# Kernel optimization log

Measured on AMD Instinct MI355X. Metric: run time of the kernel, lower is better.

Reference implementation:

```python
import jax, jax.numpy as jnp
import numpy as np

N, M, Q, H, T = 4096, 64, 64, 64, 4  # atoms, neighbors/atom, dim_q, num_neurons, num_types
BOX_L = 10.0


def setup_inputs() -> dict:
    key = jax.random.key(0)
    ks = jax.random.split(key, 7)
    return {
        "descriptors": jax.random.normal(ks[0], (N, Q), jnp.float32),
        "gradients": jax.random.normal(ks[1], (N, M, 3, Q), jnp.float32) * 0.1,
        "positions": jax.random.uniform(ks[2], (N, 3), jnp.float32) * BOX_L,
        "box": jnp.eye(3, dtype=jnp.float32) * BOX_L,
        "W0": jax.random.normal(ks[3], (T, Q, H), jnp.float32) * (1.0 / np.sqrt(Q)),
        "b0": jnp.zeros((T, H), jnp.float32),
        "W1": jax.random.normal(ks[4], (T, H), jnp.float32) * (1.0 / np.sqrt(H)),
        "Z": jax.random.randint(ks[5], (N,), 0, T, dtype=jnp.int32),
        "grad_index": jax.random.randint(ks[6], (N, M), 0, N, dtype=jnp.int32),
    }


def _pairwise_rij2(positions, box):
    """Minimum-image squared pairwise distances [N, N] (diagonal masked later)."""
    inv_box = jnp.linalg.inv(box)
    d = positions[None, :, :] - positions[:, None, :]   # [N, N, 3]
    s = d @ inv_box
    s = s - jnp.round(s)
    d = s @ box
    return jnp.sum(d * d, axis=-1)                      # [N, N] = rij^2


def reference(descriptors, gradients, positions, box, W0, b0, W1, Z, grad_index):
    n = descriptors.shape[0]
    # per-type weight gather
    W0_t = W0[Z]            # [N, Q, H]
    b0_t = b0[Z]            # [N, H]
    W1_t = W1[Z]            # [N, H]
    # hidden activations
    h = jnp.tanh(jnp.einsum('nq,nqh->nh', descriptors, W0_t) + b0_t)  # [N, H]
    # chain rule: dU_i/dq = ((1 - h^2) * W1_t) @ W0_t^T
    de_dq = jnp.einsum('nh,nqh->nq', (1.0 - h * h) * W1_t, W0_t)      # [N, Q]
    # forces: dU_i/dR_j = sum_q de_dq[i,q] * gradients[i,j,:,q]
    forces = jnp.einsum('nq,nmcq->nmc', de_dq, gradients)             # [N, M, 3]
    # pairwise squared distances with self-interaction masked out
    rij2 = _pairwise_rij2(positions, box)
    rij2 = rij2 * (1.0 - jnp.eye(n, dtype=rij2.dtype))
    # gather rij2[i, grad_index[i, m]]
    r2 = jnp.take_along_axis(rij2, grad_index.astype(jnp.int32), axis=1)  # [N, M]
    # dipole = -sum_i sum_m rij2 * force
    dipole = -jnp.sum(r2[..., None] * forces, axis=(0, 1))            # [3]
    return dipole
```

## Files before the change

### kernel.cpp

```cpp
#include <hip/hip_runtime.h>
#include <math.h>

#define QDIM 64
#define HDIM 64
#define M_NB 64
#define ATOMS_PER_BLOCK 4
#define BLOCK 256

__global__ __launch_bounds__(BLOCK) void tnep_main(
    const float* __restrict__ desc,
    const float* __restrict__ grad,
    const float* __restrict__ pos,
    const float* __restrict__ box,
    const float* __restrict__ W0,
    const float* __restrict__ b0,
    const float* __restrict__ W1,
    const int*   __restrict__ Z,
    const int*   __restrict__ gidx,
    float* __restrict__ part,
    int nblk)
{
    __shared__ __align__(16) float desc_s[ATOMS_PER_BLOCK][QDIM];
    __shared__ __align__(16) float g_s[ATOMS_PER_BLOCK][HDIM];
    __shared__ __align__(16) float de_s[ATOMS_PER_BLOCK][QDIM];
    __shared__ __align__(16) float r2_s[ATOMS_PER_BLOCK][M_NB];
    __shared__ float red_s[3][ATOMS_PER_BLOCK];

    const int tid  = threadIdx.x;
    const int w    = tid >> 6;
    const int lane = tid & 63;
    const int n    = blockIdx.x * ATOMS_PER_BLOCK + w;

    desc_s[w][lane] = desc[n * QDIM + lane];

    {
        int j = gidx[n * M_NB + lane];
        float B[9];
        #pragma unroll
        for (int k = 0; k < 9; ++k) B[k] = box[k];
        float det = B[0]*(B[4]*B[8]-B[5]*B[7])
                  - B[1]*(B[3]*B[8]-B[5]*B[6])
                  + B[2]*(B[3]*B[7]-B[4]*B[6]);
        float inv = 1.0f / det;
        float IB[9];
        IB[0] = (B[4]*B[8]-B[5]*B[7])*inv;
        IB[1] = (B[2]*B[7]-B[1]*B[8])*inv;
        IB[2] = (B[1]*B[5]-B[2]*B[4])*inv;
        IB[3] = (B[5]*B[6]-B[3]*B[8])*inv;
        IB[4] = (B[0]*B[8]-B[2]*B[6])*inv;
        IB[5] = (B[2]*B[3]-B[0]*B[5])*inv;
        IB[6] = (B[3]*B[7]-B[4]*B[6])*inv;
        IB[7] = (B[1]*B[6]-B[0]*B[7])*inv;
        IB[8] = (B[0]*B[4]-B[1]*B[3])*inv;
        float dx = pos[j*3+0] - pos[n*3+0];
        float dy = pos[j*3+1] - pos[n*3+1];
        float dz = pos[j*3+2] - pos[n*3+2];
        float sx = dx*IB[0] + dy*IB[3] + dz*IB[6];
        float sy = dx*IB[1] + dy*IB[4] + dz*IB[7];
        float sz = dx*IB[2] + dy*IB[5] + dz*IB[8];
        sx -= rintf(sx); sy -= rintf(sy); sz -= rintf(sz);
        float ex = sx*B[0] + sy*B[3] + sz*B[6];
        float ey = sx*B[1] + sy*B[4] + sz*B[7];
        float ez = sx*B[2] + sy*B[5] + sz*B[8];
        r2_s[w][lane] = ex*ex + ey*ey + ez*ez;
    }
    __syncthreads();

    const int z = Z[n];
    const float* W0t = W0 + (size_t)z * QDIM * HDIM;
    float t = b0[z * HDIM + lane];
    #pragma unroll 8
    for (int q = 0; q < QDIM; ++q)
        t += desc_s[w][q] * W0t[q * HDIM + lane];
    float ha = tanhf(t);
    g_s[w][lane] = (1.0f - ha * ha) * W1[z * HDIM + lane];
    __syncthreads();

    {
        float de = 0.0f;
        const float* W0row = W0t + lane * HDIM;
        #pragma unroll
        for (int h4 = 0; h4 < HDIM / 4; ++h4) {
            float4 wv = *(const float4*)(W0row + h4 * 4);
            float4 gv = *(const float4*)(&g_s[w][h4 * 4]);
            de += wv.x*gv.x + wv.y*gv.y + wv.z*gv.z + wv.w*gv.w;
        }
        de_s[w][lane] = de;
    }
    __syncthreads();

    float acc0 = 0.f, acc1 = 0.f, acc2 = 0.f;
    const float* base = grad + (size_t)n * M_NB * 3 * QDIM;
    #pragma unroll 4
    for (int i = 0; i < (M_NB * 3 * QDIM) / (64 * 4); ++i) {
        int f0 = (i * 64 + lane) * 4;
        float4 gv = *(const float4*)(base + f0);
        int m   = f0 / 192;
        int rem = f0 - m * 192;
        int c   = rem >> 6;
        int q0  = rem & 63;
        float4 dq = *(const float4*)(&de_s[w][q0]);
        float partial = gv.x*dq.x + gv.y*dq.y + gv.z*dq.z + gv.w*dq.w;
        float contrib = r2_s[w][m] * partial;
        acc0 += (c == 0) ? contrib : 0.f;
        acc1 += (c == 1) ? contrib : 0.f;
        acc2 += (c == 2) ? contrib : 0.f;
    }

    #pragma unroll
    for (int off = 32; off > 0; off >>= 1) {
        acc0 += __shfl_down(acc0, off, 64);
        acc1 += __shfl_down(acc1, off, 64);
        acc2 += __shfl_down(acc2, off, 64);
    }
    if (lane == 0) { red_s[0][w] = acc0; red_s[1][w] = acc1; red_s[2][w] = acc2; }
    __syncthreads();
    if (tid < 3) {
        float s = red_s[tid][0] + red_s[tid][1] + red_s[tid][2] + red_s[tid][3];
        part[tid * nblk + blockIdx.x] = s;
    }
}

__global__ __launch_bounds__(256) void tnep_reduce(
    const float* __restrict__ part, float* __restrict__ out, int nblk)
{
    __shared__ float red[256];
    int t = threadIdx.x;
    for (int c = 0; c < 3; ++c) {
        float s = 0.f;
        for (int b = t; b < nblk; b += 256) s += part[c * nblk + b];
        red[t] = s;
        __syncthreads();
        for (int off = 128; off > 0; off >>= 1) {
            if (t < off) red[t] += red[t + off];
            __syncthreads();
        }
        if (t == 0) out[c] = -red[0];
        __syncthreads();
    }
}

extern "C" void kernel_launch(void* const* d_in, const int* in_sizes, int n_in,
                              void* d_out, int out_size, void* d_ws, size_t ws_size,
                              hipStream_t stream) {
    const float* desc = (const float*)d_in[0];
    const float* grad = (const float*)d_in[1];
    const float* pos  = (const float*)d_in[2];
    const float* box  = (const float*)d_in[3];
    const float* W0   = (const float*)d_in[4];
    const float* b0   = (const float*)d_in[5];
    const float* W1   = (const float*)d_in[6];
    const int*   Z    = (const int*)d_in[7];
    const int*   gidx = (const int*)d_in[8];

    const int N    = in_sizes[0] / QDIM;
    const int nblk = N / ATOMS_PER_BLOCK;

    float* part = (float*)d_ws;

    tnep_main<<<nblk, BLOCK, 0, stream>>>(desc, grad, pos, box, W0, b0, W1,
                                          Z, gidx, part, nblk);
    tnep_reduce<<<1, 256, 0, stream>>>(part, (float*)d_out, nblk);
}
```

Measured before the change: 303.7 us.

## Split setup and gradient streaming into separate kernels with nontemporal loads

Moves the per-atom MLP and distance work into a setup kernel that writes de_dq and r2 to workspace. A second kernel then streams the large gradients tensor with a precomputed index pattern, nontemporal vector loads, and FMA-based component selection, with no dependent compute before the loads. The final reduce switches from a shared-memory tree to wave shuffles. In exchange it adds a kernel launch and a workspace round trip for the small intermediates.

Result: faster. 291.1 us (-4.2%).

```diff
diff --git a/kernel.cpp b/kernel.cpp
--- a/kernel.cpp
+++ b/kernel.cpp
@@ -4,12 +4,12 @@
 #define QDIM 64
 #define HDIM 64
 #define M_NB 64
-#define ATOMS_PER_BLOCK 4
 #define BLOCK 256
 
-__global__ __launch_bounds__(BLOCK) void tnep_main(
+typedef float f4 __attribute__((ext_vector_type(4)));
+
+__global__ __launch_bounds__(BLOCK) void tnep_setup(
     const float* __restrict__ desc,
-    const float* __restrict__ grad,
     const float* __restrict__ pos,
     const float* __restrict__ box,
     const float* __restrict__ W0,
@@ -17,19 +17,16 @@
     const float* __restrict__ W1,
     const int*   __restrict__ Z,
     const int*   __restrict__ gidx,
-    float* __restrict__ part,
-    int nblk)
+    float* __restrict__ de_out,
+    float* __restrict__ r2_out)
 {
-    __shared__ __align__(16) float desc_s[ATOMS_PER_BLOCK][QDIM];
-    __shared__ __align__(16) float g_s[ATOMS_PER_BLOCK][HDIM];
-    __shared__ __align__(16) float de_s[ATOMS_PER_BLOCK][QDIM];
-    __shared__ __align__(16) float r2_s[ATOMS_PER_BLOCK][M_NB];
-    __shared__ float red_s[3][ATOMS_PER_BLOCK];
+    __shared__ __align__(16) float desc_s[4][QDIM];
+    __shared__ __align__(16) float g_s[4][HDIM];
 
     const int tid  = threadIdx.x;
     const int w    = tid >> 6;
     const int lane = tid & 63;
-    const int n    = blockIdx.x * ATOMS_PER_BLOCK + w;
+    const int n    = blockIdx.x * 4 + w;
 
     desc_s[w][lane] = desc[n * QDIM + lane];
 
@@ -62,7 +59,7 @@
         float ex = sx*B[0] + sy*B[3] + sz*B[6];
         float ey = sx*B[1] + sy*B[4] + sz*B[7];
         float ez = sx*B[2] + sy*B[5] + sz*B[8];
-        r2_s[w][lane] = ex*ex + ey*ey + ez*ez;
+        r2_out[n * M_NB + lane] = ex*ex + ey*ey + ez*ez;
     }
     __syncthreads();
 
@@ -85,26 +82,66 @@
             float4 gv = *(const float4*)(&g_s[w][h4 * 4]);
             de += wv.x*gv.x + wv.y*gv.y + wv.z*gv.z + wv.w*gv.w;
         }
-        de_s[w][lane] = de;
+        de_out[n * QDIM + lane] = de;
     }
+}
+
+__global__ __launch_bounds__(BLOCK) void tnep_stream(
+    const float* __restrict__ grad,
+    const float* __restrict__ de,
+    const float* __restrict__ r2w,
+    float* __restrict__ part,
+    int nblk)
+{
+    __shared__ __align__(16) float r2_s[256];
+    __shared__ __align__(16) float de_s[256];
+    __shared__ float red_s[3][4];
+
+    const int t    = threadIdx.x;
+    const int blk  = blockIdx.x;
+    const int w    = t >> 6;
+    const int lane = t & 63;
+
+    r2_s[t] = r2w[blk * 256 + t];
+    de_s[t] = de[blk * 256 + t];
     __syncthreads();
 
+    const int g16 = t >> 4;
+    const int q0  = 4 * (t & 15);
+    const int gm  = g16 % 3;
+    const int m0  = g16 / 3;
+
+    float s0[3], s1[3], s2[3];
+    int   dm[3];
+    #pragma unroll
+    for (int rr = 0; rr < 3; ++rr) {
+        int c = gm + rr; if (c >= 3) c -= 3;
+        s0[rr] = (c == 0) ? 1.f : 0.f;
+        s1[rr] = (c == 1) ? 1.f : 0.f;
+        s2[rr] = (c == 2) ? 1.f : 0.f;
+        dm[rr] = 5 + ((c == 2) ? 1 : 0);
+    }
+
+    const f4* gp = (const f4*)grad + (size_t)blk * 12288 + t;
+
     float acc0 = 0.f, acc1 = 0.f, acc2 = 0.f;
-    const float* base = grad + (size_t)n * M_NB * 3 * QDIM;
-    #pragma unroll 4
-    for (int i = 0; i < (M_NB * 3 * QDIM) / (64 * 4); ++i) {
-        int f0 = (i * 64 + lane) * 4;
-        float4 gv = *(const float4*)(base + f0);
-        int m   = f0 / 192;
-        int rem = f0 - m * 192;
-        int c   = rem >> 6;
-        int q0  = rem & 63;
-        float4 dq = *(const float4*)(&de_s[w][q0]);
-        float partial = gv.x*dq.x + gv.y*dq.y + gv.z*dq.z + gv.w*dq.w;
-        float contrib = r2_s[w][m] * partial;
-        acc0 += (c == 0) ? contrib : 0.f;
-        acc1 += (c == 1) ? contrib : 0.f;
-        acc2 += (c == 2) ? contrib : 0.f;
+    #pragma unroll
+    for (int a = 0; a < 4; ++a) {
+        f4 df = *(const f4*)(&de_s[a * 64 + q0]);
+        int m = m0;
+        #pragma unroll
+        for (int ii = 0; ii < 12; ++ii) {
+            const int i = a * 12 + ii;
+            f4 gv = __builtin_nontemporal_load(gp + i * 256);
+            float r2v = r2_s[a * 64 + m];
+            float dot = gv.x*df.x + gv.y*df.y + gv.z*df.z + gv.w*df.w;
+            float contrib = r2v * dot;
+            const int rr = ii % 3;
+            acc0 = fmaf(s0[rr], contrib, acc0);
+            acc1 = fmaf(s1[rr], contrib, acc1);
+            acc2 = fmaf(s2[rr], contrib, acc2);
+            m += dm[rr];
+        }
     }
 
     #pragma unroll
@@ -115,28 +152,21 @@
     }
     if (lane == 0) { red_s[0][w] = acc0; red_s[1][w] = acc1; red_s[2][w] = acc2; }
     __syncthreads();
-    if (tid < 3) {
-        float s = red_s[tid][0] + red_s[tid][1] + red_s[tid][2] + red_s[tid][3];
-        part[tid * nblk + blockIdx.x] = s;
+    if (t < 3) {
+        part[t * nblk + blk] = red_s[t][0] + red_s[t][1] + red_s[t][2] + red_s[t][3];
     }
 }
 
 __global__ __launch_bounds__(256) void tnep_reduce(
     const float* __restrict__ part, float* __restrict__ out, int nblk)
 {
-    __shared__ float red[256];
-    int t = threadIdx.x;
-    for (int c = 0; c < 3; ++c) {
+    const int t = threadIdx.x, w = t >> 6, lane = t & 63;
+    if (w < 3) {
         float s = 0.f;
-        for (int b = t; b < nblk; b += 256) s += part[c * nblk + b];
-        red[t] = s;
-        __syncthreads();
-        for (int off = 128; off > 0; off >>= 1) {
-            if (t < off) red[t] += red[t + off];
-            __syncthreads();
-        }
-        if (t == 0) out[c] = -red[0];
-        __syncthreads();
+        for (int b = lane; b < nblk; b += 64) s += part[w * nblk + b];
+        #pragma unroll
+        for (int off = 32; off > 0; off >>= 1) s += __shfl_down(s, off, 64);
+        if (lane == 0) out[w] = -s;
     }
 }
 
@@ -154,11 +184,14 @@
     const int*   gidx = (const int*)d_in[8];
 
     const int N    = in_sizes[0] / QDIM;
-    const int nblk = N / ATOMS_PER_BLOCK;
+    const int nblk = N / 4;
 
-    float* part = (float*)d_ws;
+    float* part  = (float*)d_ws;
+    float* de_ws = (float*)d_ws + 8192;
+    float* r2_ws = de_ws + (size_t)N * 64;
 
-    tnep_main<<<nblk, BLOCK, 0, stream>>>(desc, grad, pos, box, W0, b0, W1,
-                                          Z, gidx, part, nblk);
-    tnep_reduce<<<1, 256, 0, stream>>>(part, (float*)d_out, nblk);
+    tnep_setup<<<nblk, BLOCK, 0, stream>>>(desc, pos, box, W0, b0, W1, Z, gidx,
+                                           de_ws, r2_ws);
+    tnep_stream<<<nblk, BLOCK, 0, stream>>>(grad, de_ws, r2_ws, part, nblk);
+    tnep_reduce<<<1, BLOCK, 0, stream>>>(part, (float*)d_out, nblk);
 }
```
